# Performance work log

Hardware: AMD Instinct MI355X
Metric: run time of the kernel (lower is better)

Reference implementation:

```python
import jax, jax.numpy as jnp
import numpy as np

N_UNITS = 512
H = 8
D_K = N_UNITS // H  # 64
B = 4
T = 1024


def setup_inputs() -> dict:
    key = jax.random.key(0)
    ks = jax.random.split(key, 10)
    s = 0.02
    return {
        "x": jax.random.normal(ks[0], (B * T, N_UNITS), dtype=jnp.float32),
        "pos_k": jax.random.normal(ks[1], (T, T, D_K), dtype=jnp.float32),
        "batch_size": B,
        "Wq": jax.random.normal(ks[2], (N_UNITS, N_UNITS), dtype=jnp.float32) * s,
        "bq": jax.random.normal(ks[3], (N_UNITS,), dtype=jnp.float32) * s,
        "Wk": jax.random.normal(ks[4], (N_UNITS, N_UNITS), dtype=jnp.float32) * s,
        "bk": jax.random.normal(ks[5], (N_UNITS,), dtype=jnp.float32) * s,
        "Wv": jax.random.normal(ks[6], (N_UNITS, N_UNITS), dtype=jnp.float32) * s,
        "bv": jax.random.normal(ks[7], (N_UNITS,), dtype=jnp.float32) * s,
        "Wo": jax.random.normal(ks[8], (N_UNITS, N_UNITS), dtype=jnp.float32) * s,
        "bo": jax.random.normal(ks[9], (N_UNITS,), dtype=jnp.float32) * s,
    }


def reference(x, pos_k, batch_size, Wq, bq, Wk, bk, Wv, bv, Wo, bo):
    # x: [B*T, n_units]; pos_k: [T, T, d_k]
    q = (x @ Wq + bq).reshape(batch_size, -1, H, D_K).transpose(0, 2, 1, 3)  # [B,h,T,d]
    k = (x @ Wk + bk).reshape(batch_size, -1, H, D_K).transpose(0, 2, 1, 3)
    v = (x @ Wv + bv).reshape(batch_size, -1, H, D_K).transpose(0, 2, 1, 3)
    att_score = jnp.einsum("bhqd,bhkd->bhqk", q, k)
    # relative-position score: per query position t, q[:,:,t] @ pos_k[t].T
    att_score_pos = jnp.einsum("bhqd,qkd->bhqk", q, pos_k)
    scores = (att_score + att_score_pos) / np.sqrt(D_K).astype(np.float32)
    att = jax.nn.softmax(scores, axis=3)  # dropout p=0 -> identity (eval)
    out = jnp.einsum("bhqk,bhkd->bhqd", att, v)  # [B,h,T,d]
    out = out.transpose(0, 2, 1, 3).reshape(-1, H * D_K)  # [B*T, n_units]
    return out @ Wo + bo
```

## Files before the change

kernel.cpp:

```cpp
#include <hip/hip_runtime.h>


#define TT 1024
#define DH 64
#define NH 8
#define NU 512

typedef __bf16 bf16;
typedef bf16 bf16x8 __attribute__((ext_vector_type(8)));
typedef bf16 bf16x4 __attribute__((ext_vector_type(4)));
typedef float f32x4 __attribute__((ext_vector_type(4)));

#define MFMA16(a, b, c) __builtin_amdgcn_mfma_f32_16x16x32_bf16(a, b, c, 0, 0, 0)

__global__ __launch_bounds__(256) void cvtx_k(const float* __restrict__ x,
                                              bf16* __restrict__ xb) {
  int i = blockIdx.x * 256 + threadIdx.x;
  float4 v = ((const float4*)x)[i];
  bf16x4 o = {(bf16)v.x, (bf16)v.y, (bf16)v.z, (bf16)v.w};
  ((bf16x4*)xb)[i] = o;
}

__global__ __launch_bounds__(256) void wtrans_k(const float* __restrict__ Wq,
                                                const float* __restrict__ Wk,
                                                const float* __restrict__ Wv,
                                                const float* __restrict__ Wo,
                                                bf16* __restrict__ wt) {
  int n = blockIdx.x * 256 + threadIdx.x;
  int k0 = blockIdx.y * 8;
  int w = blockIdx.z;
  const float* W = (w == 0) ? Wq : (w == 1) ? Wk : (w == 2) ? Wv : Wo;
  bf16x8 v;
#pragma unroll
  for (int j = 0; j < 8; j++) v[j] = (bf16)W[(size_t)(k0 + j) * NU + n];
  *(bf16x8*)(wt + ((size_t)w * NU + n) * NU + k0) = v;
}

__global__ __launch_bounds__(256) void qkv_k(
    const bf16* __restrict__ xb, const bf16* __restrict__ wt,
    const float* __restrict__ bq, const float* __restrict__ bk,
    const float* __restrict__ bv, bf16* __restrict__ Qb, bf16* __restrict__ Kb,
    bf16* __restrict__ Vt) {
  int tid = threadIdx.x, wid = tid >> 6, ln = tid & 63;
  int n15 = ln & 15, qd = ln >> 4;
  int n0 = blockIdx.x * 64, m0 = blockIdx.y * 64;
  int mrow = m0 + wid * 16 + n15;

  const f32x4 fz = {0.f, 0.f, 0.f, 0.f};
  f32x4 acc[3][4];
#pragma unroll
  for (int w = 0; w < 3; w++)
#pragma unroll
    for (int nt = 0; nt < 4; nt++) acc[w][nt] = fz;

  for (int k0 = 0; k0 < NU; k0 += 32) {
    bf16x8 a = *(const bf16x8*)(xb + (size_t)mrow * NU + k0 + qd * 8);
#pragma unroll
    for (int w = 0; w < 3; w++)
#pragma unroll
      for (int nt = 0; nt < 4; nt++) {
        bf16x8 b = *(const bf16x8*)(wt + ((size_t)w * NU + n0 + nt * 16 + n15) * NU +
                                    k0 + qd * 8);
        acc[w][nt] = MFMA16(a, b, acc[w][nt]);
      }
  }

  int bb = m0 >> 10;
  int tbase = (m0 & 1023) + wid * 16 + qd * 4;
  int hh = n0 >> 6;
#pragma unroll
  for (int nt = 0; nt < 4; nt++) {
    int d = nt * 16 + n15;
    float bqv = bq[n0 + d], bkv = bk[n0 + d], bvv = bv[n0 + d];
    bf16x4 vv;
#pragma unroll
    for (int r = 0; r < 4; r++) {
      int t = tbase + r;
      size_t qk_idx = ((size_t)(bb * NH + hh) * TT + t) * DH + d;
      Qb[qk_idx] = (bf16)(acc[0][nt][r] + bqv);
      Kb[qk_idx] = (bf16)(acc[1][nt][r] + bkv);
      vv[r] = (bf16)(acc[2][nt][r] + bvv);
    }
    *(bf16x4*)(Vt + ((size_t)(bb * NH + hh) * DH + d) * TT + tbase) = vv;
  }
}

__global__ __launch_bounds__(256) void pos_gemm_k(const float* __restrict__ pos,
                                                  const bf16* __restrict__ Qb,
                                                  bf16* __restrict__ biasF) {
  int tid = threadIdx.x, wid = tid >> 6, ln = tid & 63;
  int n15 = ln & 15, qd = ln >> 4;
  int t = blockIdx.y;
  int s0b = blockIdx.x * 128;

  __shared__ bf16 Qs[32 * 72];
  {
    int bh = tid >> 3, dc = (tid & 7) * 8;
    *(bf16x8*)(&Qs[bh * 72 + dc]) =
        *(const bf16x8*)(Qb + ((size_t)bh * TT + t) * DH + dc);
  }
  __syncthreads();

  bf16x8 bQ[2][2];
#pragma unroll
  for (int bht = 0; bht < 2; bht++)
#pragma unroll
    for (int kc = 0; kc < 2; kc++)
      bQ[bht][kc] = *(const bf16x8*)(&Qs[(bht * 16 + n15) * 72 + kc * 32 + qd * 8]);

  const f32x4 fz = {0.f, 0.f, 0.f, 0.f};
  f32x4 acc[2][2];
#pragma unroll
  for (int stl = 0; stl < 2; stl++)
#pragma unroll
    for (int bht = 0; bht < 2; bht++) acc[stl][bht] = fz;

  int sw = s0b + wid * 32;
#pragma unroll
  for (int stl = 0; stl < 2; stl++) {
    const float* pr = pos + ((size_t)t * TT + sw + stl * 16 + n15) * DH + qd * 8;
#pragma unroll
    for (int kc = 0; kc < 2; kc++) {
      f32x4 u = __builtin_nontemporal_load((const f32x4*)(pr + kc * 32));
      f32x4 v = __builtin_nontemporal_load((const f32x4*)(pr + kc * 32 + 4));
      bf16x8 aP = {(bf16)u[0], (bf16)u[1], (bf16)u[2], (bf16)u[3],
                   (bf16)v[0], (bf16)v[1], (bf16)v[2], (bf16)v[3]};
#pragma unroll
      for (int bht = 0; bht < 2; bht++)
        acc[stl][bht] = MFMA16(aP, bQ[bht][kc], acc[stl][bht]);
    }
  }

  int t16 = t >> 4, tin = t & 15, s32 = (s0b >> 5) + wid;
#pragma unroll
  for (int bht = 0; bht < 2; bht++) {
    bf16x8 ov;
#pragma unroll
    for (int r = 0; r < 4; r++) {
      ov[r] = (bf16)acc[0][bht][r];
      ov[4 + r] = (bf16)acc[1][bht][r];
    }
    *(bf16x8*)(biasF +
               (((size_t)(bht * 16 + n15) * 64 + t16) * 32 + s32) * 512 +
               tin * 32 + qd * 8) = ov;
  }
}

__global__ __launch_bounds__(256) void flash_k(const bf16* __restrict__ Qb,
                                               const bf16* __restrict__ Kb,
                                               const bf16* __restrict__ Vt,
                                               const bf16* __restrict__ biasF,
                                               bf16* __restrict__ att) {
  int tid = threadIdx.x, wid = tid >> 6, ln = tid & 63;
  int n15 = ln & 15, qd = ln >> 4;
  int bh = blockIdx.x;
  int t0 = blockIdx.y * 64 + wid * 16;
  const float SC = 0.18033688f;

  __shared__ bf16 Pl[4][16][40];

  bf16x8 bQ[2];
#pragma unroll
  for (int kc = 0; kc < 2; kc++)
    bQ[kc] = *(const bf16x8*)(Qb + ((size_t)bh * TT + t0 + n15) * DH + kc * 32 + qd * 8);

  const bf16* Kbase = Kb + (size_t)bh * TT * DH;
  const bf16* Vbase = Vt + (size_t)bh * DH * TT;
  const bf16* Fbase = biasF + (((size_t)bh * 64 + (t0 >> 4)) * 32) * 512 +
                      n15 * 32 + qd * 8;

  const f32x4 fz = {0.f, 0.f, 0.f, 0.f};
  f32x4 accO[4] = {fz, fz, fz, fz};
  f32x4 accL = fz;
  const bf16 one = (bf16)1.0f;
  const bf16x8 onesv = {one, one, one, one, one, one, one, one};

  bf16x8 Kf[2][4], Vf[2][4];
  bf16x8 Bf[4];

  auto ldKV = [&](int buf, int s0) {
#pragma unroll
    for (int mt = 0; mt < 2; mt++)
#pragma unroll
      for (int kc = 0; kc < 2; kc++)
        Kf[buf][mt * 2 + kc] =
            *(const bf16x8*)(Kbase + (size_t)(s0 + mt * 16 + n15) * DH + kc * 32 + qd * 8);
#pragma unroll
    for (int dt = 0; dt < 4; dt++)
      Vf[buf][dt] = *(const bf16x8*)(Vbase + (size_t)(dt * 16 + n15) * TT + s0 + qd * 8);
  };
  auto ldB = [&](int buf, int s0) {
    Bf[buf] = *(const bf16x8*)(Fbase + (size_t)(s0 >> 5) * 512);
  };

  ldB(0, 0);
  ldB(1, 32);
  ldKV(0, 0);

#pragma unroll 4
  for (int it = 0; it < 32; it++) {
    int s0 = it * 32;
    ldKV((it + 1) & 1, (s0 + 32) & 1023);
    ldB((it + 2) & 3, (s0 + 64) & 1023);

    f32x4 accS[2] = {fz, fz};
#pragma unroll
    for (int mt = 0; mt < 2; mt++)
#pragma unroll
      for (int kc = 0; kc < 2; kc++)
        accS[mt] = MFMA16(Kf[it & 1][mt * 2 + kc], bQ[kc], accS[mt]);

#pragma unroll
    for (int mt = 0; mt < 2; mt++) {
      bf16x4 pb;
#pragma unroll
      for (int r = 0; r < 4; r++) {
        float p = __builtin_amdgcn_exp2f(
            (accS[mt][r] + (float)Bf[it & 3][mt * 4 + r]) * SC);
        pb[r] = (bf16)p;
      }
      *(bf16x4*)(&Pl[wid][n15][mt * 16 + qd * 4]) = pb;
    }
    bf16x8 bP = *(const bf16x8*)(&Pl[wid][n15][qd * 8]);
    accL = MFMA16(onesv, bP, accL);
#pragma unroll
    for (int dt = 0; dt < 4; dt++) accO[dt] = MFMA16(Vf[it & 1][dt], bP, accO[dt]);
  }

  int bb = bh >> 3, hh = bh & 7;
  float rcp = 1.0f / accL[0];
#pragma unroll
  for (int dt = 0; dt < 4; dt++) {
    bf16x4 ov;
#pragma unroll
    for (int r = 0; r < 4; r++) ov[r] = (bf16)(accO[dt][r] * rcp);
    *(bf16x4*)(att + ((size_t)bb * TT + t0 + n15) * NU + hh * DH + dt * 16 + qd * 4) = ov;
  }
}

__global__ __launch_bounds__(256) void proj_k(const bf16* __restrict__ att,
                                              const bf16* __restrict__ wt,
                                              const float* __restrict__ bo,
                                              float* __restrict__ out) {
  int tid = threadIdx.x, wid = tid >> 6, ln = tid & 63;
  int n15 = ln & 15, qd = ln >> 4;
  int n0 = blockIdx.x * 64, m0 = blockIdx.y * 64;
  int mrow = m0 + wid * 16 + n15;

  const f32x4 fz = {0.f, 0.f, 0.f, 0.f};
  f32x4 acc[4] = {fz, fz, fz, fz};
  for (int k0 = 0; k0 < NU; k0 += 32) {
    bf16x8 a = *(const bf16x8*)(att + (size_t)mrow * NU + k0 + qd * 8);
#pragma unroll
    for (int nt = 0; nt < 4; nt++) {
      bf16x8 b = *(const bf16x8*)(wt + ((size_t)3 * NU + n0 + nt * 16 + n15) * NU +
                                  k0 + qd * 8);
      acc[nt] = MFMA16(a, b, acc[nt]);
    }
  }
#pragma unroll
  for (int nt = 0; nt < 4; nt++) {
    int col = n0 + nt * 16 + n15;
    float bov = bo[col];
#pragma unroll
    for (int r = 0; r < 4; r++) {
      int row = m0 + wid * 16 + qd * 4 + r;
      out[(size_t)row * NU + col] = acc[nt][r] + bov;
    }
  }
}

extern "C" void kernel_launch(void* const* d_in, const int* in_sizes, int n_in,
                              void* d_out, int out_size, void* d_ws, size_t ws_size,
                              hipStream_t stream) {
  const float* x = (const float*)d_in[0];
  const float* pos = (const float*)d_in[1];
  const float* Wq = (const float*)d_in[3];
  const float* bq = (const float*)d_in[4];
  const float* Wk = (const float*)d_in[5];
  const float* bk = (const float*)d_in[6];
  const float* Wv = (const float*)d_in[7];
  const float* bv = (const float*)d_in[8];
  const float* Wo = (const float*)d_in[9];
  const float* bo = (const float*)d_in[10];
  float* out = (float*)d_out;

  char* ws = (char*)d_ws;
  bf16* xb = (bf16*)(ws);
  bf16* wt = (bf16*)(ws + ((size_t)4 << 20));
  bf16* Qb = (bf16*)(ws + ((size_t)6 << 20));
  bf16* Kb = (bf16*)(ws + ((size_t)10 << 20));
  bf16* Vt = (bf16*)(ws + ((size_t)14 << 20));
  bf16* att = (bf16*)(ws + ((size_t)18 << 20));
  bf16* biasF = (bf16*)(ws + ((size_t)22 << 20));

  cvtx_k<<<2048, 256, 0, stream>>>(x, xb);
  wtrans_k<<<dim3(2, 64, 4), 256, 0, stream>>>(Wq, Wk, Wv, Wo, wt);
  qkv_k<<<dim3(8, 64), 256, 0, stream>>>(xb, wt, bq, bk, bv, Qb, Kb, Vt);
  pos_gemm_k<<<dim3(8, 1024), 256, 0, stream>>>(pos, Qb, biasF);
  flash_k<<<dim3(32, 16), 256, 0, stream>>>(Qb, Kb, Vt, biasF, att);
  proj_k<<<dim3(8, 64), 256, 0, stream>>>(att, wt, bo, out);
}
```

Measured before the change: 527.7 us.

## Fuse all stages into one cooperative persistent kernel with grid syncs

Replaces the six separate launches with a single cooperative kernel of 512 blocks that runs conversion, QKV projection, the positional GEMM, attention and the output projection, separated by grid-wide barriers. This removes per-launch overhead and inter-kernel gaps. In exchange, the pos GEMM stage, which is dominated by memory traffic, now runs with only 512 blocks, so each block handles two query rows instead of the wider original grid, and the grid barriers add their own cost. If the cooperative launch fails, it falls back to the original sequence of launches.

```diff
diff --git a/kernel.cpp b/kernel.cpp
--- a/kernel.cpp
+++ b/kernel.cpp
@@ -1,4 +1,7 @@
 #include <hip/hip_runtime.h>
+#include <hip/hip_cooperative_groups.h>
+
+namespace cg = cooperative_groups;
 
 
 #define TT 1024
@@ -12,6 +15,7 @@
 typedef float f32x4 __attribute__((ext_vector_type(4)));
 
 #define MFMA16(a, b, c) __builtin_amdgcn_mfma_f32_16x16x32_bf16(a, b, c, 0, 0, 0)
+
 
 __global__ __launch_bounds__(256) void cvtx_k(const float* __restrict__ x,
                                               bf16* __restrict__ xb) {
@@ -269,6 +273,271 @@
     }
   }
 }
+
+
+__global__ __launch_bounds__(256, 2) void fused_k(
+    const float* __restrict__ x, const float* __restrict__ pos,
+    const float* __restrict__ Wq, const float* __restrict__ bq,
+    const float* __restrict__ Wk, const float* __restrict__ bk,
+    const float* __restrict__ Wv, const float* __restrict__ bv,
+    const float* __restrict__ Wo, const float* __restrict__ bo,
+    bf16* __restrict__ xb, bf16* __restrict__ wt, bf16* __restrict__ Qb,
+    bf16* __restrict__ Kb, bf16* __restrict__ Vt, bf16* __restrict__ biasF,
+    bf16* __restrict__ att, float* __restrict__ out) {
+  cg::grid_group grid = cg::this_grid();
+  const int tid = threadIdx.x, bid = blockIdx.x;
+  const int wid = tid >> 6, ln = tid & 63;
+  const int n15 = ln & 15, qd = ln >> 4;
+  const f32x4 fz = {0.f, 0.f, 0.f, 0.f};
+
+  __shared__ __align__(16) bf16 smem[4608];
+
+  {
+#pragma unroll
+    for (int u = 0; u < 4; u++) {
+      int i = (u * 512 + bid) * 256 + tid;
+      float4 v = ((const float4*)x)[i];
+      bf16x4 o = {(bf16)v.x, (bf16)v.y, (bf16)v.z, (bf16)v.w};
+      ((bf16x4*)xb)[i] = o;
+    }
+    int w = bid >> 7, rem = bid & 127;
+    int k0 = (rem >> 1) * 8;
+    int n = (rem & 1) * 256 + tid;
+    const float* W = (w == 0) ? Wq : (w == 1) ? Wk : (w == 2) ? Wv : Wo;
+    bf16x8 wv;
+#pragma unroll
+    for (int j = 0; j < 8; j++) wv[j] = (bf16)W[(size_t)(k0 + j) * NU + n];
+    *(bf16x8*)(wt + ((size_t)w * NU + n) * NU + k0) = wv;
+  }
+  grid.sync();
+
+  {
+    int n0 = (bid & 7) * 64, m0 = (bid >> 3) * 64;
+    int mrow = m0 + wid * 16 + n15;
+    f32x4 acc[3][4];
+#pragma unroll
+    for (int w = 0; w < 3; w++)
+#pragma unroll
+      for (int nt = 0; nt < 4; nt++) acc[w][nt] = fz;
+
+    for (int k0 = 0; k0 < NU; k0 += 32) {
+      bf16x8 a = *(const bf16x8*)(xb + (size_t)mrow * NU + k0 + qd * 8);
+#pragma unroll
+      for (int w = 0; w < 3; w++)
+#pragma unroll
+        for (int nt = 0; nt < 4; nt++) {
+          bf16x8 b = *(const bf16x8*)(wt +
+              ((size_t)w * NU + n0 + nt * 16 + n15) * NU + k0 + qd * 8);
+          acc[w][nt] = MFMA16(a, b, acc[w][nt]);
+        }
+    }
+
+    int bb = m0 >> 10;
+    int tbase = (m0 & 1023) + wid * 16 + qd * 4;
+    int hh = n0 >> 6;
+#pragma unroll
+    for (int nt = 0; nt < 4; nt++) {
+      int d = nt * 16 + n15;
+      float bqv = bq[n0 + d], bkv = bk[n0 + d], bvv = bv[n0 + d];
+      bf16x4 vv;
+#pragma unroll
+      for (int r = 0; r < 4; r++) {
+        int t = tbase + r;
+        size_t qk_idx = ((size_t)(bb * NH + hh) * TT + t) * DH + d;
+        Qb[qk_idx] = (bf16)(acc[0][nt][r] + bqv);
+        Kb[qk_idx] = (bf16)(acc[1][nt][r] + bkv);
+        vv[r] = (bf16)(acc[2][nt][r] + bvv);
+      }
+      *(bf16x4*)(Vt + ((size_t)(bb * NH + hh) * DH + d) * TT + tbase) = vv;
+    }
+  }
+  grid.sync();
+
+  {
+    {
+      int bh = tid >> 3, dc = (tid & 7) * 8;
+#pragma unroll
+      for (int tt = 0; tt < 2; tt++) {
+        int t = bid * 2 + tt;
+        *(bf16x8*)(&smem[(size_t)(tt * 32 + bh) * 72 + dc]) =
+            *(const bf16x8*)(Qb + ((size_t)bh * TT + t) * DH + dc);
+      }
+    }
+    __syncthreads();
+
+    bf16x8 bQ2[2][2][2];
+#pragma unroll
+    for (int tt = 0; tt < 2; tt++)
+#pragma unroll
+      for (int bht = 0; bht < 2; bht++)
+#pragma unroll
+        for (int kc = 0; kc < 2; kc++)
+          bQ2[tt][bht][kc] = *(const bf16x8*)(
+              &smem[(tt * 32 + bht * 16 + n15) * 72 + kc * 32 + qd * 8]);
+
+#pragma unroll
+    for (int tt = 0; tt < 2; tt++) {
+      int t = bid * 2 + tt;
+      int t16 = t >> 4, tin = t & 15;
+#pragma unroll 2
+      for (int sc = 0; sc < 8; sc++) {
+        int sw = sc * 128 + wid * 32;
+        f32x4 acc[2][2];
+#pragma unroll
+        for (int stl = 0; stl < 2; stl++)
+#pragma unroll
+          for (int bht = 0; bht < 2; bht++) acc[stl][bht] = fz;
+
+#pragma unroll
+        for (int stl = 0; stl < 2; stl++) {
+          const float* pr =
+              pos + ((size_t)t * TT + sw + stl * 16 + n15) * DH + qd * 8;
+#pragma unroll
+          for (int kc = 0; kc < 2; kc++) {
+            f32x4 u = __builtin_nontemporal_load((const f32x4*)(pr + kc * 32));
+            f32x4 v2 = __builtin_nontemporal_load((const f32x4*)(pr + kc * 32 + 4));
+            bf16x8 aP = {(bf16)u[0], (bf16)u[1], (bf16)u[2], (bf16)u[3],
+                         (bf16)v2[0], (bf16)v2[1], (bf16)v2[2], (bf16)v2[3]};
+#pragma unroll
+            for (int bht = 0; bht < 2; bht++)
+              acc[stl][bht] = MFMA16(aP, bQ2[tt][bht][kc], acc[stl][bht]);
+          }
+        }
+
+        int s32 = sc * 4 + wid;
+#pragma unroll
+        for (int bht = 0; bht < 2; bht++) {
+          bf16x8 ov;
+#pragma unroll
+          for (int r = 0; r < 4; r++) {
+            ov[r] = (bf16)acc[0][bht][r];
+            ov[4 + r] = (bf16)acc[1][bht][r];
+          }
+          *(bf16x8*)(biasF +
+                     (((size_t)(bht * 16 + n15) * 64 + t16) * 32 + s32) * 512 +
+                     tin * 32 + qd * 8) = ov;
+        }
+      }
+    }
+  }
+  grid.sync();
+
+  {
+    int bh = bid & 31;
+    int t0 = (bid >> 5) * 64 + wid * 16;
+    const float SC = 0.18033688f;
+
+    bf16* Pl = &smem[wid * 640];
+
+    bf16x8 bQ[2];
+#pragma unroll
+    for (int kc = 0; kc < 2; kc++)
+      bQ[kc] = *(const bf16x8*)(Qb + ((size_t)bh * TT + t0 + n15) * DH +
+                                kc * 32 + qd * 8);
+
+    const bf16* Kbase = Kb + (size_t)bh * TT * DH;
+    const bf16* Vbase = Vt + (size_t)bh * DH * TT;
+    const bf16* Fbase = biasF + (((size_t)bh * 64 + (t0 >> 4)) * 32) * 512 +
+                        n15 * 32 + qd * 8;
+
+    f32x4 accO[4] = {fz, fz, fz, fz};
+    f32x4 accL = fz;
+    const bf16 one = (bf16)1.0f;
+    const bf16x8 onesv = {one, one, one, one, one, one, one, one};
+
+    bf16x8 Kf[2][4], Vf[2][4];
+    bf16x8 Bf[4];
+
+    auto ldKV = [&](int buf, int s0) {
+#pragma unroll
+      for (int mt = 0; mt < 2; mt++)
+#pragma unroll
+        for (int kc = 0; kc < 2; kc++)
+          Kf[buf][mt * 2 + kc] = *(const bf16x8*)(
+              Kbase + (size_t)(s0 + mt * 16 + n15) * DH + kc * 32 + qd * 8);
+#pragma unroll
+      for (int dt = 0; dt < 4; dt++)
+        Vf[buf][dt] =
+            *(const bf16x8*)(Vbase + (size_t)(dt * 16 + n15) * TT + s0 + qd * 8);
+    };
+    auto ldB = [&](int buf, int s0) {
+      Bf[buf] = *(const bf16x8*)(Fbase + (size_t)(s0 >> 5) * 512);
+    };
+
+    ldB(0, 0);
+    ldB(1, 32);
+    ldKV(0, 0);
+
+#pragma unroll 4
+    for (int it = 0; it < 32; it++) {
+      int s0 = it * 32;
+      ldKV((it + 1) & 1, (s0 + 32) & 1023);
+      ldB((it + 2) & 3, (s0 + 64) & 1023);
+
+      f32x4 accS[2] = {fz, fz};
+#pragma unroll
+      for (int mt = 0; mt < 2; mt++)
+#pragma unroll
+        for (int kc = 0; kc < 2; kc++)
+          accS[mt] = MFMA16(Kf[it & 1][mt * 2 + kc], bQ[kc], accS[mt]);
+
+#pragma unroll
+      for (int mt = 0; mt < 2; mt++) {
+        bf16x4 pb;
+#pragma unroll
+        for (int r = 0; r < 4; r++) {
+          float p = __builtin_amdgcn_exp2f(
+              (accS[mt][r] + (float)Bf[it & 3][mt * 4 + r]) * SC);
+          pb[r] = (bf16)p;
+        }
+        *(bf16x4*)(&Pl[n15 * 40 + mt * 16 + qd * 4]) = pb;
+      }
+      bf16x8 bP = *(const bf16x8*)(&Pl[n15 * 40 + qd * 8]);
+      accL = MFMA16(onesv, bP, accL);
+#pragma unroll
+      for (int dt = 0; dt < 4; dt++)
+        accO[dt] = MFMA16(Vf[it & 1][dt], bP, accO[dt]);
+    }
+
+    int bb = bh >> 3, hh = bh & 7;
+    float rcp = 1.0f / accL[0];
+#pragma unroll
+    for (int dt = 0; dt < 4; dt++) {
+      bf16x4 ov;
+#pragma unroll
+      for (int r = 0; r < 4; r++) ov[r] = (bf16)(accO[dt][r] * rcp);
+      *(bf16x4*)(att + ((size_t)bb * TT + t0 + n15) * NU + hh * DH + dt * 16 +
+                 qd * 4) = ov;
+    }
+  }
+  grid.sync();
+
+  {
+    int n0 = (bid & 7) * 64, m0 = (bid >> 3) * 64;
+    int mrow = m0 + wid * 16 + n15;
+    f32x4 acc[4] = {fz, fz, fz, fz};
+    for (int k0 = 0; k0 < NU; k0 += 32) {
+      bf16x8 a = *(const bf16x8*)(att + (size_t)mrow * NU + k0 + qd * 8);
+#pragma unroll
+      for (int nt = 0; nt < 4; nt++) {
+        bf16x8 b = *(const bf16x8*)(wt + ((size_t)3 * NU + n0 + nt * 16 + n15) * NU +
+                                    k0 + qd * 8);
+        acc[nt] = MFMA16(a, b, acc[nt]);
+      }
+    }
+#pragma unroll
+    for (int nt = 0; nt < 4; nt++) {
+      int col = n0 + nt * 16 + n15;
+      float bov = bo[col];
+#pragma unroll
+      for (int r = 0; r < 4; r++) {
+        int row = m0 + wid * 16 + qd * 4 + r;
+        out[(size_t)row * NU + col] = acc[nt][r] + bov;
+      }
+    }
+  }
+}
+
 
 extern "C" void kernel_launch(void* const* d_in, const int* in_sizes, int n_in,
                               void* d_out, int out_size, void* d_ws, size_t ws_size,
@@ -294,10 +563,16 @@
   bf16* att = (bf16*)(ws + ((size_t)18 << 20));
   bf16* biasF = (bf16*)(ws + ((size_t)22 << 20));
 
-  cvtx_k<<<2048, 256, 0, stream>>>(x, xb);
-  wtrans_k<<<dim3(2, 64, 4), 256, 0, stream>>>(Wq, Wk, Wv, Wo, wt);
-  qkv_k<<<dim3(8, 64), 256, 0, stream>>>(xb, wt, bq, bk, bv, Qb, Kb, Vt);
-  pos_gemm_k<<<dim3(8, 1024), 256, 0, stream>>>(pos, Qb, biasF);
-  flash_k<<<dim3(32, 16), 256, 0, stream>>>(Qb, Kb, Vt, biasF, att);
-  proj_k<<<dim3(8, 64), 256, 0, stream>>>(att, wt, bo, out);
-}
+  void* args[] = {&x,  &pos, &Wq, &bq, &Wk, &bk,    &Wv,  &bv, &Wo,
+                  &bo, &xb,  &wt, &Qb, &Kb, &Vt, &biasF, &att, &out};
+  hipError_t err = hipLaunchCooperativeKernel((void*)fused_k, dim3(512),
+                                              dim3(256), args, 0, stream);
+  if (err != hipSuccess) {
+    cvtx_k<<<2048, 256, 0, stream>>>(x, xb);
+    wtrans_k<<<dim3(2, 64, 4), 256, 0, stream>>>(Wq, Wk, Wv, Wo, wt);
+    qkv_k<<<dim3(8, 64), 256, 0, stream>>>(xb, wt, bq, bk, bv, Qb, Kb, Vt);
+    pos_gemm_k<<<dim3(8, 1024), 256, 0, stream>>>(pos, Qb, biasF);
+    flash_k<<<dim3(32, 16), 256, 0, stream>>>(Qb, Kb, Vt, biasF, att);
+    proj_k<<<dim3(8, 64), 256, 0, stream>>>(att, wt, bo, out);
+  }
+}
```

After: 798.4 us. +51.3%, slower.

## Merge prep kernels and widen flash attention key tile to 64

Applied to the files above, without the earlier changes.

Combines the x conversion and weight transpose into one prep kernel to drop a launch. The flash kernel now processes 64 keys per iteration instead of 32, with double-buffered K/V/bias register fragments, a larger LDS P tile, and launch bounds requesting two blocks per CU. This halves loop iterations and gives more MFMA work per softmax stage, at the cost of higher register pressure. The total is dominated by pos_gemm, which streams the 256MB pos_k tensor, so the gain is likely small.

```diff
diff --git a/kernel.cpp b/kernel.cpp
--- a/kernel.cpp
+++ b/kernel.cpp
@@ -13,27 +13,31 @@
 
 #define MFMA16(a, b, c) __builtin_amdgcn_mfma_f32_16x16x32_bf16(a, b, c, 0, 0, 0)
 
-__global__ __launch_bounds__(256) void cvtx_k(const float* __restrict__ x,
-                                              bf16* __restrict__ xb) {
-  int i = blockIdx.x * 256 + threadIdx.x;
-  float4 v = ((const float4*)x)[i];
-  bf16x4 o = {(bf16)v.x, (bf16)v.y, (bf16)v.z, (bf16)v.w};
-  ((bf16x4*)xb)[i] = o;
-}
-
-__global__ __launch_bounds__(256) void wtrans_k(const float* __restrict__ Wq,
-                                                const float* __restrict__ Wk,
-                                                const float* __restrict__ Wv,
-                                                const float* __restrict__ Wo,
-                                                bf16* __restrict__ wt) {
-  int n = blockIdx.x * 256 + threadIdx.x;
-  int k0 = blockIdx.y * 8;
-  int w = blockIdx.z;
-  const float* W = (w == 0) ? Wq : (w == 1) ? Wk : (w == 2) ? Wv : Wo;
-  bf16x8 v;
-#pragma unroll
-  for (int j = 0; j < 8; j++) v[j] = (bf16)W[(size_t)(k0 + j) * NU + n];
-  *(bf16x8*)(wt + ((size_t)w * NU + n) * NU + k0) = v;
+__global__ __launch_bounds__(256) void prep_k(const float* __restrict__ x,
+                                              const float* __restrict__ Wq,
+                                              const float* __restrict__ Wk,
+                                              const float* __restrict__ Wv,
+                                              const float* __restrict__ Wo,
+                                              bf16* __restrict__ xb,
+                                              bf16* __restrict__ wt) {
+  int bid = blockIdx.x, tid = threadIdx.x;
+  {
+    int i = bid * 256 + tid;
+    float4 v = ((const float4*)x)[i];
+    bf16x4 o = {(bf16)v.x, (bf16)v.y, (bf16)v.z, (bf16)v.w};
+    ((bf16x4*)xb)[i] = o;
+  }
+  if ((bid & 3) == 0) {
+    int u = bid >> 2;
+    int w = u >> 7, rem = u & 127;
+    int k0 = (rem >> 1) * 8;
+    int n = (rem & 1) * 256 + tid;
+    const float* W = (w == 0) ? Wq : (w == 1) ? Wk : (w == 2) ? Wv : Wo;
+    bf16x8 v;
+#pragma unroll
+    for (int j = 0; j < 8; j++) v[j] = (bf16)W[(size_t)(k0 + j) * NU + n];
+    *(bf16x8*)(wt + ((size_t)w * NU + n) * NU + k0) = v;
+  }
 }
 
 __global__ __launch_bounds__(256) void qkv_k(
@@ -146,18 +150,18 @@
   }
 }
 
-__global__ __launch_bounds__(256) void flash_k(const bf16* __restrict__ Qb,
-                                               const bf16* __restrict__ Kb,
-                                               const bf16* __restrict__ Vt,
-                                               const bf16* __restrict__ biasF,
-                                               bf16* __restrict__ att) {
+__global__ __launch_bounds__(256, 2) void flash_k(const bf16* __restrict__ Qb,
+                                                  const bf16* __restrict__ Kb,
+                                                  const bf16* __restrict__ Vt,
+                                                  const bf16* __restrict__ biasF,
+                                                  bf16* __restrict__ att) {
   int tid = threadIdx.x, wid = tid >> 6, ln = tid & 63;
   int n15 = ln & 15, qd = ln >> 4;
   int bh = blockIdx.x;
   int t0 = blockIdx.y * 64 + wid * 16;
   const float SC = 0.18033688f;
 
-  __shared__ bf16 Pl[4][16][40];
+  __shared__ bf16 Pl[4][16][72];
 
   bf16x8 bQ[2];
 #pragma unroll
@@ -175,56 +179,66 @@
   const bf16 one = (bf16)1.0f;
   const bf16x8 onesv = {one, one, one, one, one, one, one, one};
 
-  bf16x8 Kf[2][4], Vf[2][4];
-  bf16x8 Bf[4];
+  bf16x8 Kf[2][8], Vf[2][8];
+  bf16x8 Bf[2][2];
 
   auto ldKV = [&](int buf, int s0) {
 #pragma unroll
-    for (int mt = 0; mt < 2; mt++)
+    for (int mt = 0; mt < 4; mt++)
 #pragma unroll
       for (int kc = 0; kc < 2; kc++)
         Kf[buf][mt * 2 + kc] =
             *(const bf16x8*)(Kbase + (size_t)(s0 + mt * 16 + n15) * DH + kc * 32 + qd * 8);
 #pragma unroll
     for (int dt = 0; dt < 4; dt++)
-      Vf[buf][dt] = *(const bf16x8*)(Vbase + (size_t)(dt * 16 + n15) * TT + s0 + qd * 8);
+#pragma unroll
+      for (int sc = 0; sc < 2; sc++)
+        Vf[buf][dt * 2 + sc] =
+            *(const bf16x8*)(Vbase + (size_t)(dt * 16 + n15) * TT + s0 + sc * 32 + qd * 8);
   };
   auto ldB = [&](int buf, int s0) {
-    Bf[buf] = *(const bf16x8*)(Fbase + (size_t)(s0 >> 5) * 512);
+#pragma unroll
+    for (int sc = 0; sc < 2; sc++)
+      Bf[buf][sc] = *(const bf16x8*)(Fbase + (size_t)((s0 >> 5) + sc) * 512);
   };
 
+  ldKV(0, 0);
   ldB(0, 0);
-  ldB(1, 32);
-  ldKV(0, 0);
-
-#pragma unroll 4
-  for (int it = 0; it < 32; it++) {
-    int s0 = it * 32;
-    ldKV((it + 1) & 1, (s0 + 32) & 1023);
-    ldB((it + 2) & 3, (s0 + 64) & 1023);
-
-    f32x4 accS[2] = {fz, fz};
-#pragma unroll
-    for (int mt = 0; mt < 2; mt++)
+
+#pragma unroll 2
+  for (int it = 0; it < 16; it++) {
+    int s0 = it * 64;
+    int cb = it & 1, nb = (it + 1) & 1;
+    ldKV(nb, (s0 + 64) & 1023);
+    ldB(nb, (s0 + 64) & 1023);
+
+    f32x4 accS[4] = {fz, fz, fz, fz};
+#pragma unroll
+    for (int mt = 0; mt < 4; mt++)
 #pragma unroll
       for (int kc = 0; kc < 2; kc++)
-        accS[mt] = MFMA16(Kf[it & 1][mt * 2 + kc], bQ[kc], accS[mt]);
-
-#pragma unroll
-    for (int mt = 0; mt < 2; mt++) {
+        accS[mt] = MFMA16(Kf[cb][mt * 2 + kc], bQ[kc], accS[mt]);
+
+#pragma unroll
+    for (int mt = 0; mt < 4; mt++) {
       bf16x4 pb;
 #pragma unroll
       for (int r = 0; r < 4; r++) {
         float p = __builtin_amdgcn_exp2f(
-            (accS[mt][r] + (float)Bf[it & 3][mt * 4 + r]) * SC);
+            (accS[mt][r] + (float)Bf[cb][mt >> 1][(mt & 1) * 4 + r]) * SC);
         pb[r] = (bf16)p;
       }
       *(bf16x4*)(&Pl[wid][n15][mt * 16 + qd * 4]) = pb;
     }
-    bf16x8 bP = *(const bf16x8*)(&Pl[wid][n15][qd * 8]);
-    accL = MFMA16(onesv, bP, accL);
-#pragma unroll
-    for (int dt = 0; dt < 4; dt++) accO[dt] = MFMA16(Vf[it & 1][dt], bP, accO[dt]);
+
+#pragma unroll
+    for (int sc = 0; sc < 2; sc++) {
+      bf16x8 bP = *(const bf16x8*)(&Pl[wid][n15][sc * 32 + qd * 8]);
+      accL = MFMA16(onesv, bP, accL);
+#pragma unroll
+      for (int dt = 0; dt < 4; dt++)
+        accO[dt] = MFMA16(Vf[cb][dt * 2 + sc], bP, accO[dt]);
+    }
   }
 
   int bb = bh >> 3, hh = bh & 7;
@@ -294,8 +308,7 @@
   bf16* att = (bf16*)(ws + ((size_t)18 << 20));
   bf16* biasF = (bf16*)(ws + ((size_t)22 << 20));
 
-  cvtx_k<<<2048, 256, 0, stream>>>(x, xb);
-  wtrans_k<<<dim3(2, 64, 4), 256, 0, stream>>>(Wq, Wk, Wv, Wo, wt);
+  prep_k<<<2048, 256, 0, stream>>>(x, Wq, Wk, Wv, Wo, xb, wt);
   qkv_k<<<dim3(8, 64), 256, 0, stream>>>(xb, wt, bq, bk, bv, Qb, Kb, Vt);
   pos_gemm_k<<<dim3(8, 1024), 256, 0, stream>>>(pos, Qb, biasF);
   flash_k<<<dim3(32, 16), 256, 0, stream>>>(Qb, Kb, Vt, biasF, att);
```

After: 527.7 us. Within noise of the previous version (-0.0%).
